# Kernel tuning notes

Hardware: AMD Instinct MI355X
Metric: run time of the kernel (lower is better)

## Reference

```python
import jax, jax.numpy as jnp
import numpy as np

# Ragged per-tensor sequence lengths (dim 1 of each input)
_LENS = [64, 128, 192, 256, 320, 384, 448, 512]
_B = 512   # batch size
_D = 128   # feature dim


def setup_inputs() -> dict:
    key = jax.random.key(0)
    keys = jax.random.split(key, len(_LENS))
    return {
        f"x{i}": jax.random.normal(keys[i], (_B, L, _D), dtype=jnp.float32)
        for i, L in enumerate(_LENS)
    }


def reference(x0, x1, x2, x3, x4, x5, x6, x7) -> jnp.ndarray:
    # Fused sum-over-seq + concat: equivalent to
    # torch.cat([t.sum(dim=1, keepdim=True) for t in inputs], dim=1)
    # (keep_dims=True, cat_axis=1 path -> mlu_triton_fuse_sum_cat_3d).
    inputs = (x0, x1, x2, x3, x4, x5, x6, x7)
    # Each summand is [B, 1, D]; output is [B, N, D] with N = len(inputs).
    return jnp.concatenate([t.sum(axis=1, keepdims=True) for t in inputs], axis=1)
```

## Files before the change

kernel.cpp:

```cpp
#include <hip/hip_runtime.h>


struct SumCatArgs {
    const float* x[8];
    int L[8];
};

__global__ __launch_bounds__(256) void fuse_sum_cat_kernel(
    SumCatArgs args, float* __restrict__ out) {
    const int wid  = threadIdx.x >> 6;
    const int lane = threadIdx.x & 63;

    const int bk = blockIdx.x;
    const int b  = bk >> 1;
    const int p  = (bk & 1) * 2 + (wid >> 1);
    const int i  = (wid & 1) ? (7 - p) : p;
    const int L  = args.L[i];

    const float4* __restrict__ xr =
        (const float4*)args.x[i] + (size_t)b * (size_t)L * 32;

    float4 a0 = make_float4(0.f, 0.f, 0.f, 0.f);
    float4 a1 = make_float4(0.f, 0.f, 0.f, 0.f);

    for (int lb = 0; lb < L; lb += 16) {
        const float4* __restrict__ w = xr + (size_t)lb * 32;
        float4 v[8];
#pragma unroll
        for (int u = 0; u < 8; ++u) v[u] = w[u * 64 + lane];
#pragma unroll
        for (int u = 0; u < 8; u += 2) {
            a0.x += v[u].x;     a0.y += v[u].y;
            a0.z += v[u].z;     a0.w += v[u].w;
            a1.x += v[u + 1].x; a1.y += v[u + 1].y;
            a1.z += v[u + 1].z; a1.w += v[u + 1].w;
        }
    }

    float4 acc = make_float4(a0.x + a1.x, a0.y + a1.y,
                             a0.z + a1.z, a0.w + a1.w);

    acc.x += __shfl_down(acc.x, 32, 64);
    acc.y += __shfl_down(acc.y, 32, 64);
    acc.z += __shfl_down(acc.z, 32, 64);
    acc.w += __shfl_down(acc.w, 32, 64);

    if (lane < 32) {
        float4* __restrict__ orow =
            (float4*)(out + ((size_t)b * 8 + i) * 128);
        orow[lane] = acc;
    }
}

extern "C" void kernel_launch(void* const* d_in, const int* in_sizes, int n_in,
                              void* d_out, int out_size, void* d_ws, size_t ws_size,
                              hipStream_t stream) {
    (void)d_ws; (void)ws_size; (void)out_size; (void)n_in;

    SumCatArgs args;
    for (int i = 0; i < 8; ++i) {
        args.x[i] = (const float*)d_in[i];
        args.L[i] = in_sizes[i] / (512 * 128);
    }

    fuse_sum_cat_kernel<<<1024, 256, 0, stream>>>(args, (float*)d_out);
}
```

Baseline: 485.6 us.

## Balance row work evenly across waves with shared-memory atomic segment reduction

Each block's four tensors are concatenated into one virtual row range of 1152 rows, split evenly into 288-row slices per wave, so the waves no longer get unequal work from the ragged lengths. Partial sums are combined with LDS atomics and written out after a barrier. Loads are double-buffered with sched_barrier to keep more memory requests in flight. This adds LDS atomics, two __syncthreads, and hardcodes the 288-row split to the fixed total length.

```diff
diff --git a/kernel.cpp b/kernel.cpp
--- a/kernel.cpp
+++ b/kernel.cpp
@@ -6,50 +6,108 @@
     int L[8];
 };
 
-__global__ __launch_bounds__(256) void fuse_sum_cat_kernel(
+__device__ __forceinline__ void load_chunk(float4 (&v)[8],
+                                           const float4* __restrict__ base,
+                                           int c, int lane) {
+#pragma unroll
+    for (int u = 0; u < 8; ++u)
+        v[u] = base[(size_t)c * 512 + u * 64 + lane];
+    __builtin_amdgcn_sched_barrier(0);
+}
+
+__device__ __forceinline__ void acc_chunk(float4& p0, float4& p1,
+                                          const float4 (&v)[8]) {
+#pragma unroll
+    for (int u = 0; u < 8; u += 2) {
+        p0.x += v[u].x;     p0.y += v[u].y;
+        p0.z += v[u].z;     p0.w += v[u].w;
+        p1.x += v[u + 1].x; p1.y += v[u + 1].y;
+        p1.z += v[u + 1].z; p1.w += v[u + 1].w;
+    }
+}
+
+__global__ __launch_bounds__(256, 4) void fuse_sum_cat_kernel(
     SumCatArgs args, float* __restrict__ out) {
+    const int lane = threadIdx.x & 63;
     const int wid  = threadIdx.x >> 6;
-    const int lane = threadIdx.x & 63;
+    const int bk   = blockIdx.x;
+    const int b    = bk >> 1;
+    const int h    = bk & 1;
 
-    const int bk = blockIdx.x;
-    const int b  = bk >> 1;
-    const int p  = (bk & 1) * 2 + (wid >> 1);
-    const int i  = (wid & 1) ? (7 - p) : p;
-    const int L  = args.L[i];
+    __shared__ float oacc[4][128];
+    ((float2*)&oacc[0][0])[threadIdx.x] = make_float2(0.f, 0.f);
+    __syncthreads();
 
-    const float4* __restrict__ xr =
-        (const float4*)args.x[i] + (size_t)b * (size_t)L * 32;
+    const int t0 = h ? 2 : 0, t1 = h ? 5 : 7, t2 = h ? 3 : 1, t3 = h ? 4 : 6;
+    const float* __restrict__ xp0 = h ? args.x[2] : args.x[0];
+    const float* __restrict__ xp1 = h ? args.x[5] : args.x[7];
+    const float* __restrict__ xp2 = h ? args.x[3] : args.x[1];
+    const float* __restrict__ xp3 = h ? args.x[4] : args.x[6];
+    const int L0 = h ? args.L[2] : args.L[0];
+    const int L1 = h ? args.L[5] : args.L[7];
+    const int L2 = h ? args.L[3] : args.L[1];
+    const int L3 = h ? args.L[4] : args.L[6];
 
-    float4 a0 = make_float4(0.f, 0.f, 0.f, 0.f);
-    float4 a1 = make_float4(0.f, 0.f, 0.f, 0.f);
+    const int pre1 = L0, pre2 = pre1 + L1, pre3 = pre2 + L2, pre4 = pre3 + L3;
 
-    for (int lb = 0; lb < L; lb += 16) {
-        const float4* __restrict__ w = xr + (size_t)lb * 32;
-        float4 v[8];
-#pragma unroll
-        for (int u = 0; u < 8; ++u) v[u] = w[u * 64 + lane];
-#pragma unroll
-        for (int u = 0; u < 8; u += 2) {
-            a0.x += v[u].x;     a0.y += v[u].y;
-            a0.z += v[u].z;     a0.w += v[u].w;
-            a1.x += v[u + 1].x; a1.y += v[u + 1].y;
-            a1.z += v[u + 1].z; a1.w += v[u + 1].w;
-        }
+    const int r0 = wid * 288;
+    const int r1 = r0 + 288;
+
+#define PROCESS_SEG(S, XP, LS, PS, PE)                                        \
+    {                                                                         \
+        const int lo = r0 > (PS) ? r0 : (PS);                                 \
+        const int hi = r1 < (PE) ? r1 : (PE);                                 \
+        if (hi > lo) {                                                        \
+            const float4* __restrict__ base =                                 \
+                (const float4*)(XP) +                                         \
+                ((size_t)b * (size_t)(LS) + (size_t)(lo - (PS))) * 32;        \
+            const int n = (hi - lo) >> 4;                                     \
+            float4 A[8], B[8];                                                \
+            float4 p0 = make_float4(0.f, 0.f, 0.f, 0.f);                      \
+            float4 p1 = make_float4(0.f, 0.f, 0.f, 0.f);                      \
+            load_chunk(A, base, 0, lane);                                     \
+            int c = 1;                                                        \
+            for (; c + 1 < n; c += 2) {                                       \
+                load_chunk(B, base, c, lane);                                 \
+                acc_chunk(p0, p1, A);                                         \
+                load_chunk(A, base, c + 1, lane);                             \
+                acc_chunk(p0, p1, B);                                         \
+            }                                                                 \
+            if (c < n) {                                                      \
+                load_chunk(B, base, c, lane);                                 \
+                acc_chunk(p0, p1, A);                                         \
+                acc_chunk(p0, p1, B);                                         \
+            } else {                                                          \
+                acc_chunk(p0, p1, A);                                         \
+            }                                                                 \
+            float4 acc = make_float4(p0.x + p1.x, p0.y + p1.y,                \
+                                     p0.z + p1.z, p0.w + p1.w);               \
+            acc.x += __shfl_down(acc.x, 32, 64);                              \
+            acc.y += __shfl_down(acc.y, 32, 64);                              \
+            acc.z += __shfl_down(acc.z, 32, 64);                              \
+            acc.w += __shfl_down(acc.w, 32, 64);                              \
+            if (lane < 32) {                                                  \
+                atomicAdd(&oacc[S][lane * 4 + 0], acc.x);                     \
+                atomicAdd(&oacc[S][lane * 4 + 1], acc.y);                     \
+                atomicAdd(&oacc[S][lane * 4 + 2], acc.z);                     \
+                atomicAdd(&oacc[S][lane * 4 + 3], acc.w);                     \
+            }                                                                 \
+        }                                                                     \
     }
 
-    float4 acc = make_float4(a0.x + a1.x, a0.y + a1.y,
-                             a0.z + a1.z, a0.w + a1.w);
+    PROCESS_SEG(0, xp0, L0, 0,    pre1)
+    PROCESS_SEG(1, xp1, L1, pre1, pre2)
+    PROCESS_SEG(2, xp2, L2, pre2, pre3)
+    PROCESS_SEG(3, xp3, L3, pre3, pre4)
+#undef PROCESS_SEG
 
-    acc.x += __shfl_down(acc.x, 32, 64);
-    acc.y += __shfl_down(acc.y, 32, 64);
-    acc.z += __shfl_down(acc.z, 32, 64);
-    acc.w += __shfl_down(acc.w, 32, 64);
+    __syncthreads();
 
-    if (lane < 32) {
-        float4* __restrict__ orow =
-            (float4*)(out + ((size_t)b * 8 + i) * 128);
-        orow[lane] = acc;
-    }
+    const int rl = wid;
+    const int d  = lane * 2;
+    const int ti = rl == 0 ? t0 : rl == 1 ? t1 : rl == 2 ? t2 : t3;
+    float2 v = *(const float2*)&oacc[rl][d];
+    *(float2*)&out[((size_t)b * 8 + ti) * 128 + d] = v;
 }
 
 extern "C" void kernel_launch(void* const* d_in, const int* in_sizes, int n_in,
```

Result: no change. 485.2 us (-0.1%).
